# Kernel tuning notes

Hardware: AMD Instinct MI355X
Metric: run time of the kernel (lower is better)

The kernel has to match this reference:

```python
import jax, jax.numpy as jnp
import numpy as np
from jax import lax

DIM, HEADS, WS = 256, 8, 8
B, H, W = 2, 192, 192


def conv1x1(x, w, b):
    # x: (b,c,h,w), w: (o,c)
    return jnp.einsum('bchw,oc->bohw', x, w) + b[None, :, None, None]


def dwconv3x3(x, w, b):
    # w: (C,1,3,3), zeros padding (padding_mode='zeros')
    y = lax.conv_general_dilated(x, w, (1, 1), ((1, 1), (1, 1)),
                                 dimension_numbers=('NCHW', 'OIHW', 'NCHW'),
                                 feature_group_count=x.shape[1])
    return y + b[None, :, None, None]


def window_split(qkv):
    # (b, 3*heads*c, H, W) -> (3, b*h1*w1, heads, c, ws*ws)
    b, C3, h, w = qkv.shape
    c = C3 // (3 * HEADS)
    h1, w1 = h // WS, w // WS
    t = qkv.reshape(b, 3, HEADS, c, h1, WS, w1, WS)
    t = t.transpose(1, 0, 4, 6, 2, 3, 5, 7)  # (3,b,h1,w1,heads,c,ws,ws)
    return t.reshape(3, b * h1 * w1, HEADS, c, WS * WS)


def window_merge(o, b, h, w):
    # (b*h1*w1, heads, c, ws*ws) -> (b, heads*c, h, w)
    h1, w1 = h // WS, w // WS
    c = o.shape[2]
    t = o.reshape(b, h1, w1, HEADS, c, WS, WS)
    t = t.transpose(0, 3, 4, 1, 5, 2, 6)  # (b,heads,c,h1,ws,w1,ws)
    return t.reshape(b, HEADS * c, h, w)


def l2norm(x):
    n = jnp.linalg.norm(x, axis=-1, keepdims=True)
    return x / jnp.maximum(n, 1e-12)


def setup_inputs() -> dict:
    key = jax.random.key(0)
    ks = jax.random.split(key, 16)
    s = 0.02
    return {
        'x': jax.random.normal(ks[0], (B, DIM, H, W), jnp.float32),
        'x2': jax.random.normal(ks[1], (B, DIM, H, W), jnp.float32),
        'w_qkv': jax.random.normal(ks[2], (3 * DIM, DIM), jnp.float32) * s,
        'b_qkv': jnp.zeros((3 * DIM,), jnp.float32),
        'w_dw': jax.random.normal(ks[3], (3 * DIM, 1, 3, 3), jnp.float32) * s,
        'b_dw': jnp.zeros((3 * DIM,), jnp.float32),
        'w_qkv2': jax.random.normal(ks[4], (3 * DIM, DIM), jnp.float32) * s,
        'b_qkv2': jnp.zeros((3 * DIM,), jnp.float32),
        'w_dw2': jax.random.normal(ks[5], (3 * DIM, 1, 3, 3), jnp.float32) * s,
        'b_dw2': jnp.zeros((3 * DIM,), jnp.float32),
        'temp': jnp.ones((HEADS, 1, 1), jnp.float32) / np.sqrt(DIM).astype(np.float32),
        'w_proj': jax.random.normal(ks[6], (DIM, DIM), jnp.float32) * s,
        'b_proj': jnp.zeros((DIM,), jnp.float32),
    }


def reference(x, x2, w_qkv, b_qkv, w_dw, b_dw, w_qkv2, b_qkv2, w_dw2, b_dw2,
              temp, w_proj, b_proj):
    b, _, h, w = x.shape
    qkv = dwconv3x3(conv1x1(x, w_qkv, b_qkv), w_dw, b_dw)
    qkv2 = dwconv3x3(conv1x1(x2, w_qkv2, b_qkv2), w_dw2, b_dw2)
    # H,W divisible by window_size -> check_image_size is a no-op
    q, k, v = window_split(qkv)       # each (Bw, heads, c, N)
    q2, k2, v2 = window_split(qkv2)
    q, k = l2norm(q), l2norm(k)
    q2, k2 = l2norm(q2), l2norm(k2)
    # channel attention (cs='channel'): scores are (c x c) per window/head
    cross = jnp.einsum('whcn,whdn->whcd', q, k2) * temp  # q @ k2^T
    cross = jax.nn.softmax(cross, axis=-1)
    cross_out = jnp.einsum('whcd,whdn->whcn', cross, v2)
    out = window_merge(cross_out, b, h, w)
    return conv1x1(out, w_proj, b_proj)
```

## Files before the change

### kernel.cpp

```cpp
#include <hip/hip_runtime.h>
#include <stdint.h>

typedef unsigned short u16;
typedef __attribute__((ext_vector_type(4))) unsigned short u16x4;
typedef __attribute__((ext_vector_type(8))) short bf16x8;
typedef __attribute__((ext_vector_type(4))) float f32x4;

#define PTOT 36864
#define WIMG 192

__device__ __forceinline__ float bf2f(u16 h) {
    union { uint32_t u; float f; } v; v.u = ((uint32_t)h) << 16; return v.f;
}
__device__ __forceinline__ u16 f2bf(float f) {
    union { float f; uint32_t u; } v; v.f = f;
    uint32_t u = v.u;
    return (u16)((u + 0x7FFFu + ((u >> 16) & 1u)) >> 16);
}

#define ASYNC_COPY16(gp, lp)                                                     \
    __builtin_amdgcn_global_load_lds(                                            \
        (const __attribute__((address_space(1))) void*)(gp),                     \
        (__attribute__((address_space(3))) void*)(lp), 16, 0, 0)

__global__ __launch_bounds__(256) void k_transpose(const float* __restrict__ x,
                                                   const float* __restrict__ x2,
                                                   u16* __restrict__ xt,
                                                   u16* __restrict__ x2t) {
    __shared__ u16 tile[64][66];
    const int tx = threadIdx.x, ty = threadIdx.y;
    const int p0 = blockIdx.x * 64, c0 = blockIdx.y * 64;
    const int z = blockIdx.z, b = z & 1;
    const float* src = (z < 2 ? x : x2) + (size_t)b * 256 * PTOT;
    u16* dst = (z < 2 ? xt : x2t) + (size_t)b * PTOT * 256;
#pragma unroll
    for (int k = 0; k < 16; ++k) {
        const int c = c0 + ty + k * 4;
        tile[ty + k * 4][tx] = f2bf(src[(size_t)c * PTOT + p0 + tx]);
    }
    __syncthreads();
#pragma unroll
    for (int k = 0; k < 16; ++k) {
        const int p = p0 + ty + k * 4;
        dst[(size_t)p * 256 + c0 + tx] = tile[tx][ty + k * 4];
    }
}

__global__ void k_f2bfAll(const float* __restrict__ w_qkv,
                          const float* __restrict__ w_qkv2,
                          const float* __restrict__ w_proj,
                          u16* __restrict__ dst) {
    const int i = blockIdx.x * 256 + threadIdx.x;
    float v;
    if (i < 65536) v = w_qkv[i];
    else if (i < 196608) v = w_qkv2[i];
    else v = w_proj[i - 196608];
    dst[i] = f2bf(v);
}

template <bool OUT_F32>
__global__ __launch_bounds__(256) void k_gemm(const u16* __restrict__ A,
                                              const u16* __restrict__ Bt,
                                              void* __restrict__ Cout,
                                              const float* __restrict__ bias,
                                              int M) {
    __shared__ u16 As[128 * 32];
    __shared__ u16 Bs[128 * 32];
    const int tid = threadIdx.x;
    const int lane = tid & 63;
    const int wave = tid >> 6;
    const int wr = wave >> 1, wc = wave & 1;
    const int nb = blockIdx.x, mb = blockIdx.y, b = blockIdx.z;

    const u16* Ab = A + (size_t)(mb * 128) * 256;
    const u16* Bb = Bt + ((size_t)b * PTOT + (size_t)nb * 128) * 256;

    const int lrow = lane >> 2;
    const int lcol = (lane & 3) * 8;
    const int lr = lane & 15;
    const int lk = lane >> 4;

    f32x4 acc[4][4];
#pragma unroll
    for (int m = 0; m < 4; ++m)
#pragma unroll
        for (int n = 0; n < 4; ++n) acc[m][n] = (f32x4)0.f;

    for (int k0 = 0; k0 < 256; k0 += 32) {
        __syncthreads();
        const int i0 = wave * 2;
#pragma unroll
        for (int ii = 0; ii < 2; ++ii) {
            const int i = i0 + ii;
            ASYNC_COPY16(Ab + (size_t)(i * 16 + lrow) * 256 + k0 + lcol,
                         As + i * 16 * 32);
            ASYNC_COPY16(Bb + (size_t)(i * 16 + lrow) * 256 + k0 + lcol,
                         Bs + i * 16 * 32);
        }
        __syncthreads();
        const bf16x8* Asv = (const bf16x8*)As;
        const bf16x8* Bsv = (const bf16x8*)Bs;
        bf16x8 afr[4], bfr[4];
#pragma unroll
        for (int m = 0; m < 4; ++m)
            afr[m] = Asv[(wr * 64 + m * 16 + lr) * 4 + lk];
#pragma unroll
        for (int n = 0; n < 4; ++n)
            bfr[n] = Bsv[(wc * 64 + n * 16 + lr) * 4 + lk];
#pragma unroll
        for (int m = 0; m < 4; ++m)
#pragma unroll
            for (int n = 0; n < 4; ++n)
                acc[m][n] = __builtin_amdgcn_mfma_f32_16x16x32_bf16(
                    afr[m], bfr[n], acc[m][n], 0, 0, 0);
    }

    const int cr = (lane >> 4) * 4;
    const int cc = lane & 15;
#pragma unroll
    for (int m = 0; m < 4; ++m) {
#pragma unroll
        for (int j = 0; j < 4; ++j) {
            const int row = mb * 128 + wr * 64 + m * 16 + cr + j;
            const float bv = bias[row];
            const size_t rbase =
                ((size_t)b * M + row) * PTOT + (size_t)nb * 128 + wc * 64 + cc;
#pragma unroll
            for (int n = 0; n < 4; ++n) {
                const float v = acc[m][n][j] + bv;
                if (OUT_F32)
                    ((float*)Cout)[rbase + n * 16] = v;
                else
                    ((u16*)Cout)[rbase + n * 16] = f2bf(v);
            }
        }
    }
}

__global__ __launch_bounds__(256) void k_dwfrag(const u16* __restrict__ qpre,
                                                const u16* __restrict__ kvpre,
                                                const float* __restrict__ w_dw,
                                                const float* __restrict__ b_dw,
                                                const float* __restrict__ w_dw2,
                                                const float* __restrict__ b_dw2,
                                                u16* __restrict__ qw,
                                                u16* __restrict__ kw,
                                                u16* __restrict__ vw) {
    const int tid = threadIdx.x;
    const int c = tid >> 3, pxg = tid & 7;
    const int bx3 = blockIdx.x % 3, wy = blockIdx.x / 3;
    const int slab = blockIdx.y, b = blockIdx.z;
    const int path = slab >> 3, hh = slab & 7;
    const int ch = hh * 32 + c;

    const u16* src;
    const float* wp;
    float bias;
    u16* dst;
    if (path == 0) {
        src = qpre + ((size_t)b * 256 + ch) * PTOT;
        wp = w_dw + ch * 9; bias = b_dw[ch]; dst = qw;
    } else if (path == 1) {
        src = kvpre + ((size_t)b * 512 + ch) * PTOT;
        wp = w_dw2 + (256 + ch) * 9; bias = b_dw2[256 + ch]; dst = kw;
    } else {
        src = kvpre + ((size_t)b * 512 + 256 + ch) * PTOT;
        wp = w_dw2 + (512 + ch) * 9; bias = b_dw2[512 + ch]; dst = vw;
    }
    float w9[9];
#pragma unroll
    for (int i = 0; i < 9; ++i) w9[i] = wp[i];

    const int x0 = bx3 * 64 + pxg * 8;
    const size_t winbase =
        (((size_t)b * 8 + hh) * 576 + (size_t)wy * 24 + bx3 * 8 + pxg) * 2048;
    const int gy0 = wy * 8;

    float pr[4][10];
#define LOADROW(SLOT, YY)                                                        \
    do {                                                                         \
        const int yy_ = (YY);                                                    \
        if ((unsigned)yy_ >= (unsigned)WIMG) {                                   \
            _Pragma("unroll") for (int i_ = 0; i_ < 10; ++i_) pr[SLOT][i_] = 0.f;\
        } else {                                                                 \
            const u16* row_ = src + (size_t)yy_ * WIMG + x0;                     \
            const bf16x8 cv_ = *(const bf16x8*)row_;                             \
            pr[SLOT][0] = (x0 > 0) ? bf2f(row_[-1]) : 0.f;                       \
            pr[SLOT][9] = (x0 < 184) ? bf2f(row_[8]) : 0.f;                      \
            _Pragma("unroll") for (int i_ = 0; i_ < 8; ++i_)                     \
                pr[SLOT][i_ + 1] = bf2f((u16)cv_[i_]);                           \
        }                                                                        \
    } while (0)

    LOADROW(0, gy0 - 1);
    LOADROW(1, gy0);
    LOADROW(2, gy0 + 1);

#pragma unroll
    for (int y = 0; y < 8; ++y) {
        if (y < 7) LOADROW((y + 3) & 3, gy0 + y + 2);
        const int s0 = y & 3, s1 = (y + 1) & 3, s2 = (y + 2) & 3;
        float acc[8];
#pragma unroll
        for (int i = 0; i < 8; ++i)
            acc[i] = bias
                   + w9[0] * pr[s0][i] + w9[1] * pr[s0][i + 1] + w9[2] * pr[s0][i + 2]
                   + w9[3] * pr[s1][i] + w9[4] * pr[s1][i + 1] + w9[5] * pr[s1][i + 2]
                   + w9[6] * pr[s2][i] + w9[7] * pr[s2][i + 1] + w9[8] * pr[s2][i + 2];
        bf16x8 ov;
#pragma unroll
        for (int i = 0; i < 8; ++i) ov[i] = (short)f2bf(acc[i]);
        *(bf16x8*)(dst + winbase + y * 256 + c * 8) = ov;
    }
#undef LOADROW
}

__global__ __launch_bounds__(256) void k_attn(const u16* __restrict__ qw,
                                              const u16* __restrict__ kw,
                                              const u16* __restrict__ vw,
                                              const float* __restrict__ temp,
                                              u16* __restrict__ outt) {
    __shared__ __align__(16) char lds[28160];
    float* SS = (float*)lds;
    u16* P = (u16*)(lds + 16896);
    float* IQ = (float*)(lds + 27136);
    float* IK = (float*)(lds + 27648);

    const int tid = threadIdx.x;
    const int lane = tid & 63;
    const int wv = tid >> 6;
    const int h = blockIdx.y, b = blockIdx.z;
    const int win_lin = blockIdx.x * 4 + wv;
    const int wy = win_lin / 24, wxc = win_lin % 24;
    const int lr = lane & 15, lk = lane >> 4;

    const size_t fb = (((size_t)b * 8 + h) * 576 + win_lin) * 2048;

    bf16x8 aq[2][2], bk[2][2], vb[4];
#pragma unroll
    for (int kb = 0; kb < 2; ++kb) {
        const int roff = (kb * 4 + lk) * 256;
#pragma unroll
        for (int half = 0; half < 2; ++half) {
            const int coff = (half * 16 + lr) * 8;
            aq[kb][half] = *(const bf16x8*)(qw + fb + roff + coff);
            bk[kb][half] = *(const bf16x8*)(kw + fb + roff + coff);
        }
    }
#pragma unroll
    for (int ni = 0; ni < 4; ++ni) {
        const int n = ni * 16 + lr;
        const u16* vsrc = vw + fb + (size_t)(n >> 3) * 256 + (n & 7);
        bf16x8 v;
#pragma unroll
        for (int j = 0; j < 8; ++j) v[j] = (short)vsrc[(lk * 8 + j) * 8];
        vb[ni] = v;
    }

    {
        float sq0 = 0.f, sq1 = 0.f, sk0 = 0.f, sk1 = 0.f;
#pragma unroll
        for (int kb = 0; kb < 2; ++kb)
#pragma unroll
            for (int j = 0; j < 8; ++j) {
                float a0 = bf2f((u16)aq[kb][0][j]), a1 = bf2f((u16)aq[kb][1][j]);
                float k0 = bf2f((u16)bk[kb][0][j]), k1 = bf2f((u16)bk[kb][1][j]);
                sq0 += a0 * a0; sq1 += a1 * a1;
                sk0 += k0 * k0; sk1 += k1 * k1;
            }
        sq0 += __shfl_xor(sq0, 16); sq0 += __shfl_xor(sq0, 32);
        sq1 += __shfl_xor(sq1, 16); sq1 += __shfl_xor(sq1, 32);
        sk0 += __shfl_xor(sk0, 16); sk0 += __shfl_xor(sk0, 32);
        sk1 += __shfl_xor(sk1, 16); sk1 += __shfl_xor(sk1, 32);
        if (lk == 0) {
            IQ[wv * 32 + lr]      = 1.f / fmaxf(sqrtf(sq0), 1e-12f);
            IQ[wv * 32 + 16 + lr] = 1.f / fmaxf(sqrtf(sq1), 1e-12f);
            IK[wv * 32 + lr]      = 1.f / fmaxf(sqrtf(sk0), 1e-12f);
            IK[wv * 32 + 16 + lr] = 1.f / fmaxf(sqrtf(sk1), 1e-12f);
        }
    }

    {
        f32x4 s00 = (f32x4)0.f, s01 = (f32x4)0.f, s10 = (f32x4)0.f, s11 = (f32x4)0.f;
#pragma unroll
        for (int kb = 0; kb < 2; ++kb) {
            s00 = __builtin_amdgcn_mfma_f32_16x16x32_bf16(aq[kb][0], bk[kb][0], s00, 0, 0, 0);
            s01 = __builtin_amdgcn_mfma_f32_16x16x32_bf16(aq[kb][0], bk[kb][1], s01, 0, 0, 0);
            s10 = __builtin_amdgcn_mfma_f32_16x16x32_bf16(aq[kb][1], bk[kb][0], s10, 0, 0, 0);
            s11 = __builtin_amdgcn_mfma_f32_16x16x32_bf16(aq[kb][1], bk[kb][1], s11, 0, 0, 0);
        }
        float* srow = SS + wv * 1056;
        const int cr = lk * 4, cc = lr;
#pragma unroll
        for (int j = 0; j < 4; ++j) {
            srow[(cr + j) * 33 + cc] = s00[j];
            srow[(cr + j) * 33 + 16 + cc] = s01[j];
            srow[(16 + cr + j) * 33 + cc] = s10[j];
            srow[(16 + cr + j) * 33 + 16 + cc] = s11[j];
        }
    }
    __syncthreads();

    if (lane < 32) {
        const float* srow = SS + wv * 1056 + lane * 33;
        const float* ik = IK + wv * 32;
        const float iq = IQ[wv * 32 + lane] * temp[h];
        float sv[32];
        float mx = -1e30f;
#pragma unroll
        for (int d = 0; d < 32; ++d) {
            sv[d] = srow[d] * ik[d] * iq;
            mx = fmaxf(mx, sv[d]);
        }
        float sum = 0.f;
#pragma unroll
        for (int d = 0; d < 32; ++d) {
            sv[d] = __expf(sv[d] - mx);
            sum += sv[d];
        }
        const float pinv = 1.f / sum;
        u16* prow = P + wv * 1280 + lane * 40;
#pragma unroll
        for (int ch = 0; ch < 4; ++ch) {
            bf16x8 pv;
#pragma unroll
            for (int i = 0; i < 8; ++i) pv[i] = (short)f2bf(sv[ch * 8 + i] * pinv);
            *(bf16x8*)(prow + ch * 8) = pv;
        }
    }
    __syncthreads();

    {
        bf16x8 pa0 = *(const bf16x8*)(P + wv * 1280 + lr * 40 + lk * 8);
        bf16x8 pa1 = *(const bf16x8*)(P + wv * 1280 + (16 + lr) * 40 + lk * 8);
        f32x4 o0[4], o1[4];
#pragma unroll
        for (int ni = 0; ni < 4; ++ni) { o0[ni] = (f32x4)0.f; o1[ni] = (f32x4)0.f; }
#pragma unroll
        for (int ni = 0; ni < 4; ++ni) {
            o0[ni] = __builtin_amdgcn_mfma_f32_16x16x32_bf16(pa0, vb[ni], o0[ni], 0, 0, 0);
            o1[ni] = __builtin_amdgcn_mfma_f32_16x16x32_bf16(pa1, vb[ni], o1[ni], 0, 0, 0);
        }
#pragma unroll
        for (int ni = 0; ni < 4; ++ni) {
            const int n = ni * 16 + lr;
            const size_t gp = (size_t)(wy * 8 + (n >> 3)) * WIMG + wxc * 8 + (n & 7);
            u16* op = outt + ((size_t)b * PTOT + gp) * 256 + h * 32;
            u16x4 pk0, pk1;
#pragma unroll
            for (int j = 0; j < 4; ++j) { pk0[j] = f2bf(o0[ni][j]); pk1[j] = f2bf(o1[ni][j]); }
            *(u16x4*)(op + lk * 4) = pk0;
            *(u16x4*)(op + 16 + lk * 4) = pk1;
        }
    }
}

extern "C" void kernel_launch(void* const* d_in, const int* in_sizes, int n_in,
                              void* d_out, int out_size, void* d_ws, size_t ws_size,
                              hipStream_t stream) {
    (void)in_sizes; (void)n_in; (void)out_size; (void)ws_size;
    const float* x      = (const float*)d_in[0];
    const float* x2     = (const float*)d_in[1];
    const float* w_qkv  = (const float*)d_in[2];
    const float* b_qkv  = (const float*)d_in[3];
    const float* w_dw   = (const float*)d_in[4];
    const float* b_dw   = (const float*)d_in[5];
    const float* w_qkv2 = (const float*)d_in[6];
    const float* b_qkv2 = (const float*)d_in[7];
    const float* w_dw2  = (const float*)d_in[8];
    const float* b_dw2  = (const float*)d_in[9];
    const float* temp   = (const float*)d_in[10];
    const float* w_proj = (const float*)d_in[11];
    const float* b_proj = (const float*)d_in[12];
    float* out = (float*)d_out;

    char* ws = (char*)d_ws;
    const size_t SZ_T  = (size_t)2 * PTOT * 256 * 2;
    const size_t SZ_KV = (size_t)2 * PTOT * 512 * 2;
    u16* xt     = (u16*)(ws);
    u16* x2t    = (u16*)(ws + SZ_T);
    u16* qpre   = (u16*)(ws + 2 * SZ_T);
    u16* kvpre  = (u16*)(ws + 3 * SZ_T);
    u16* vw     = (u16*)(ws + 3 * SZ_T + SZ_KV);
    u16* wq     = (u16*)(ws + 4 * SZ_T + SZ_KV);
    u16* wkv    = wq + 256 * 256;
    u16* wproj  = wkv + 512 * 256;
    u16* qw     = xt;
    u16* kw     = x2t;
    u16* attnt  = qpre;

    const dim3 tb(64, 4);
    k_transpose<<<dim3(PTOT / 64, 4, 4), tb, 0, stream>>>(x, x2, xt, x2t);
    k_f2bfAll<<<262144 / 256, 256, 0, stream>>>(w_qkv, w_qkv2, w_proj, wq);

    k_gemm<false><<<dim3(PTOT / 128, 2, 2), 256, 0, stream>>>(wq, xt, qpre, b_qkv, 256);
    k_gemm<false><<<dim3(PTOT / 128, 4, 2), 256, 0, stream>>>(wkv, x2t, kvpre, b_qkv2 + 256, 512);

    k_dwfrag<<<dim3(72, 24, 2), 256, 0, stream>>>(qpre, kvpre, w_dw, b_dw,
                                                  w_dw2, b_dw2, qw, kw, vw);

    k_attn<<<dim3(144, 8, 2), 256, 0, stream>>>(qw, kw, vw, temp, attnt);

    k_gemm<true><<<dim3(PTOT / 128, 2, 2), 256, 0, stream>>>(wproj, attnt, out, b_proj, 256);
}
```

Measured before the change: 219.7 us.

## Fuse fp32-to-bf16 input transpose into QKV GEMM B-tile loading

Removes the separate transpose/convert kernel for x and x2. The QKV GEMMs now read the fp32 NCHW inputs directly, convert them to bf16 in registers and write them transposed into a padded LDS tile. This drops one kernel launch and the write and re-read of the bf16 transposed intermediate. In exchange, the GEMM reads fp32 (twice the bytes), and does so once per M-block (two or four times over). These loads are synchronous and not overlapped with the MFMA work.

New measurement: 226.4 us. +3.1%, slower.

```diff
diff --git a/kernel.cpp b/kernel.cpp
--- a/kernel.cpp
+++ b/kernel.cpp
@@ -22,29 +22,6 @@
     __builtin_amdgcn_global_load_lds(                                            \
         (const __attribute__((address_space(1))) void*)(gp),                     \
         (__attribute__((address_space(3))) void*)(lp), 16, 0, 0)
-
-__global__ __launch_bounds__(256) void k_transpose(const float* __restrict__ x,
-                                                   const float* __restrict__ x2,
-                                                   u16* __restrict__ xt,
-                                                   u16* __restrict__ x2t) {
-    __shared__ u16 tile[64][66];
-    const int tx = threadIdx.x, ty = threadIdx.y;
-    const int p0 = blockIdx.x * 64, c0 = blockIdx.y * 64;
-    const int z = blockIdx.z, b = z & 1;
-    const float* src = (z < 2 ? x : x2) + (size_t)b * 256 * PTOT;
-    u16* dst = (z < 2 ? xt : x2t) + (size_t)b * PTOT * 256;
-#pragma unroll
-    for (int k = 0; k < 16; ++k) {
-        const int c = c0 + ty + k * 4;
-        tile[ty + k * 4][tx] = f2bf(src[(size_t)c * PTOT + p0 + tx]);
-    }
-    __syncthreads();
-#pragma unroll
-    for (int k = 0; k < 16; ++k) {
-        const int p = p0 + ty + k * 4;
-        dst[(size_t)p * 256 + c0 + tx] = tile[tx][ty + k * 4];
-    }
-}
 
 __global__ void k_f2bfAll(const float* __restrict__ w_qkv,
                           const float* __restrict__ w_qkv2,
@@ -58,14 +35,15 @@
     dst[i] = f2bf(v);
 }
 
-template <bool OUT_F32>
+template <bool BT_F32, bool OUT_F32>
 __global__ __launch_bounds__(256) void k_gemm(const u16* __restrict__ A,
-                                              const u16* __restrict__ Bt,
+                                              const void* __restrict__ Bsrc,
                                               void* __restrict__ Cout,
                                               const float* __restrict__ bias,
                                               int M) {
+    constexpr int BSTR = BT_F32 ? 40 : 32;
     __shared__ u16 As[128 * 32];
-    __shared__ u16 Bs[128 * 32];
+    __shared__ u16 Bs[128 * BSTR];
     const int tid = threadIdx.x;
     const int lane = tid & 63;
     const int wave = tid >> 6;
@@ -73,13 +51,15 @@
     const int nb = blockIdx.x, mb = blockIdx.y, b = blockIdx.z;
 
     const u16* Ab = A + (size_t)(mb * 128) * 256;
-    const u16* Bb = Bt + ((size_t)b * PTOT + (size_t)nb * 128) * 256;
 
     const int lrow = lane >> 2;
     const int lcol = (lane & 3) * 8;
     const int lr = lane & 15;
     const int lk = lane >> 4;
 
+    const int spx = tid & 127;
+    const int sch = (tid >> 7) * 16;
+
     f32x4 acc[4][4];
 #pragma unroll
     for (int m = 0; m < 4; ++m)
@@ -94,19 +74,37 @@
             const int i = i0 + ii;
             ASYNC_COPY16(Ab + (size_t)(i * 16 + lrow) * 256 + k0 + lcol,
                          As + i * 16 * 32);
-            ASYNC_COPY16(Bb + (size_t)(i * 16 + lrow) * 256 + k0 + lcol,
-                         Bs + i * 16 * 32);
+            if (!BT_F32)
+                ASYNC_COPY16((const u16*)Bsrc +
+                                 ((size_t)b * PTOT + (size_t)nb * 128 + i * 16 + lrow) * 256 +
+                                 k0 + lcol,
+                             Bs + i * 16 * 32);
+        }
+        if (BT_F32) {
+            const float* Bf = (const float*)Bsrc + (size_t)b * 256 * PTOT +
+                              (size_t)nb * 128 + spx;
+            float fv[16];
+#pragma unroll
+            for (int j = 0; j < 16; ++j)
+                fv[j] = Bf[(size_t)(k0 + sch + j) * PTOT];
+            bf16x8 h0, h1;
+#pragma unroll
+            for (int j = 0; j < 8; ++j) {
+                h0[j] = (short)f2bf(fv[j]);
+                h1[j] = (short)f2bf(fv[8 + j]);
+            }
+            *(bf16x8*)(Bs + spx * BSTR + sch) = h0;
+            *(bf16x8*)(Bs + spx * BSTR + sch + 8) = h1;
         }
         __syncthreads();
         const bf16x8* Asv = (const bf16x8*)As;
-        const bf16x8* Bsv = (const bf16x8*)Bs;
         bf16x8 afr[4], bfr[4];
 #pragma unroll
         for (int m = 0; m < 4; ++m)
             afr[m] = Asv[(wr * 64 + m * 16 + lr) * 4 + lk];
 #pragma unroll
         for (int n = 0; n < 4; ++n)
-            bfr[n] = Bsv[(wc * 64 + n * 16 + lr) * 4 + lk];
+            bfr[n] = *(const bf16x8*)(Bs + (wc * 64 + n * 16 + lr) * BSTR + lk * 8);
 #pragma unroll
         for (int m = 0; m < 4; ++m)
 #pragma unroll
@@ -377,29 +375,28 @@
     char* ws = (char*)d_ws;
     const size_t SZ_T  = (size_t)2 * PTOT * 256 * 2;
     const size_t SZ_KV = (size_t)2 * PTOT * 512 * 2;
-    u16* xt     = (u16*)(ws);
-    u16* x2t    = (u16*)(ws + SZ_T);
-    u16* qpre   = (u16*)(ws + 2 * SZ_T);
-    u16* kvpre  = (u16*)(ws + 3 * SZ_T);
+    u16* qpre   = (u16*)(ws);
+    u16* kvpre  = (u16*)(ws + SZ_T);
+    u16* qw     = (u16*)(ws + SZ_T + SZ_KV);
+    u16* kw     = (u16*)(ws + 2 * SZ_T + SZ_KV);
     u16* vw     = (u16*)(ws + 3 * SZ_T + SZ_KV);
     u16* wq     = (u16*)(ws + 4 * SZ_T + SZ_KV);
     u16* wkv    = wq + 256 * 256;
     u16* wproj  = wkv + 512 * 256;
-    u16* qw     = xt;
-    u16* kw     = x2t;
     u16* attnt  = qpre;
 
-    const dim3 tb(64, 4);
-    k_transpose<<<dim3(PTOT / 64, 4, 4), tb, 0, stream>>>(x, x2, xt, x2t);
     k_f2bfAll<<<262144 / 256, 256, 0, stream>>>(w_qkv, w_qkv2, w_proj, wq);
 
-    k_gemm<false><<<dim3(PTOT / 128, 2, 2), 256, 0, stream>>>(wq, xt, qpre, b_qkv, 256);
-    k_gemm<false><<<dim3(PTOT / 128, 4, 2), 256, 0, stream>>>(wkv, x2t, kvpre, b_qkv2 + 256, 512);
+    k_gemm<true, false><<<dim3(PTOT / 128, 2, 2), 256, 0, stream>>>(
+        wq, (const void*)x, qpre, b_qkv, 256);
+    k_gemm<true, false><<<dim3(PTOT / 128, 4, 2), 256, 0, stream>>>(
+        wkv, (const void*)x2, kvpre, b_qkv2 + 256, 512);
 
     k_dwfrag<<<dim3(72, 24, 2), 256, 0, stream>>>(qpre, kvpre, w_dw, b_dw,
                                                   w_dw2, b_dw2, qw, kw, vw);
 
     k_attn<<<dim3(144, 8, 2), 256, 0, stream>>>(qw, kw, vw, temp, attnt);
 
-    k_gemm<true><<<dim3(PTOT / 128, 2, 2), 256, 0, stream>>>(wproj, attnt, out, b_proj, 256);
-}
+    k_gemm<false, true><<<dim3(PTOT / 128, 2, 2), 256, 0, stream>>>(
+        wproj, (const void*)attnt, out, b_proj, 256);
+}
```
